# Optimization experiments

Hardware: AMD Instinct MI355X
Metric: run time of the kernel (lower is better)

Reference implementation:

```python
import jax, jax.numpy as jnp
import numpy as np

B, H, W, DIM = 8, 128, 128, 96
MED = 2 * DIM            # med_channels
NS = 3                   # num_scales
SCTX = 48                # spatial context channels
RIN = DIM + SCTX         # reweight mlp input
RHID = int(0.25 * RIN)   # 36
ROUT = NS * MED          # 576
FH, FWH = H, W // 2 + 1  # rfft2 output grid
SCALE_HW = [(16, 9), (8, 4), (24, 13)]  # per-scale filter resolutions


def _cubic(t, a=-0.75):
    t = abs(t)
    if t <= 1.0:
        return (a + 2) * t ** 3 - (a + 3) * t ** 2 + 1.0
    if t < 2.0:
        return a * t ** 3 - 5 * a * t ** 2 + 8 * a * t - 4 * a
    return 0.0


def _resize_mat(old, new):
    # bicubic, align_corners=True, border replication (matches F.interpolate)
    M = np.zeros((new, old), dtype=np.float32)
    for j in range(new):
        s = j * (old - 1) / (new - 1) if new > 1 else 0.0
        f = int(np.floor(s))
        for k in range(-1, 3):
            M[j, min(max(f + k, 0), old - 1)] += _cubic(s - (f + k))
    return jnp.asarray(M)


def _soa(x, scale, bias):
    r = jnp.maximum(x, 0.0)
    return scale * r * r + bias


def setup_inputs() -> dict:
    key = jax.random.key(0)
    ks = jax.random.split(key, 10)
    inp = {
        "x": jax.random.normal(ks[0], (B, H, W, DIM), dtype=jnp.float32),
        "w1": jax.random.normal(ks[1], (MED, DIM), dtype=jnp.float32) * 0.02,
        "soa1_scale": jnp.ones((1,), jnp.float32),
        "soa1_bias": jnp.zeros((1,), jnp.float32),
        "cw0": jax.random.normal(ks[2], (SCALE_HW[0][0], SCALE_HW[0][1], MED, 2), dtype=jnp.float32) * 0.02,
        "cw1": jax.random.normal(ks[3], (SCALE_HW[1][0], SCALE_HW[1][1], MED, 2), dtype=jnp.float32) * 0.02,
        "cw2": jax.random.normal(ks[4], (SCALE_HW[2][0], SCALE_HW[2][1], MED, 2), dtype=jnp.float32) * 0.02,
        "sp_w": jax.random.normal(ks[5], (SCTX, DIM), dtype=jnp.float32) * 0.05,
        "bn_gamma": jnp.ones((SCTX,), jnp.float32),
        "bn_beta": jnp.zeros((SCTX,), jnp.float32),
        "bn_mean": jnp.zeros((SCTX,), jnp.float32),
        "bn_var": jnp.ones((SCTX,), jnp.float32),
        "fc1": jax.random.normal(ks[6], (RHID, RIN), dtype=jnp.float32) * 0.05,
        "mlp_scale": jnp.ones((1,), jnp.float32),
        "mlp_bias": jnp.zeros((1,), jnp.float32),
        "fc2": jax.random.normal(ks[7], (ROUT, RHID), dtype=jnp.float32) * 0.05,
        "w2": jax.random.normal(ks[8], (DIM, MED), dtype=jnp.float32) * 0.02,
    }
    return inp


def reference(x, w1, soa1_scale, soa1_bias, cw0, cw1, cw2, sp_w,
              bn_gamma, bn_beta, bn_mean, bn_var,
              fc1, mlp_scale, mlp_bias, fc2, w2):
    # pwconv1 + Soa act
    x_pre = _soa(jnp.einsum('bhwc,mc->bhwm', x, w1), soa1_scale, soa1_bias)
    # rfft2 over spatial dims (ortho) -> [B, FH, FWH, MED] complex64
    xf = jnp.fft.rfft2(x_pre.transpose(0, 3, 1, 2), axes=(2, 3), norm='ortho').transpose(0, 2, 3, 1)
    # resize each scale's complex weight to the fft grid (bicubic align_corners=True)
    filts = []
    for cw in (cw0, cw1, cw2):
        Rh = _resize_mat(cw.shape[0], FH)
        Rw = _resize_mat(cw.shape[1], FWH)
        t = jnp.einsum('Hh,hwmc->Hwmc', Rh, cw)
        t = jnp.einsum('Ww,Hwmc->HWmc', Rw, t)
        filts.append(jax.lax.complex(t[..., 0], t[..., 1]))
    filt = jnp.stack(filts)  # [NS, FH, FWH, MED] complex64
    # routing context: global channel mean + 1x1 conv / BN(eval) / relu / GAP
    gctx = x.mean(axis=(1, 2))  # [B, DIM]
    y = jnp.einsum('bhwc,sc->bhws', x, sp_w)
    y = (y - bn_mean) * jax.lax.rsqrt(bn_var + 1e-5) * bn_gamma + bn_beta
    sctx = jnp.maximum(y, 0.0).mean(axis=(1, 2))  # [B, SCTX]
    fused = jnp.concatenate([gctx, sctx], axis=1)  # [B, RIN]
    hmid = _soa(fused @ fc1.T, mlp_scale, mlp_bias)
    r = jax.nn.softmax((hmid @ fc2.T).reshape(-1, NS, MED), axis=1)  # [B, NS, MED]
    # routing-weighted combined filter + spectral multiply
    comb = jnp.einsum('shwm,bsm->bhwm', filt, r.astype(filt.dtype))
    xff = xf * comb
    xsp = jnp.fft.irfft2(xff.transpose(0, 3, 1, 2), s=(H, W), axes=(2, 3), norm='ortho').transpose(0, 2, 3, 1)
    # act2 is Identity; pwconv2
    return jnp.einsum('bhwm,cm->bhwc', xsp, w2)
```

## Files before the change

kernel.cpp:

```cpp
#include <hip/hip_runtime.h>
#include <math.h>

#define BB    8
#define HH    128
#define WW    128
#define DIM   96
#define MED   192
#define HWPX  16384
#define FWH   65
#define LSTR  67

#define P_OFF     0
#define P_SZ      (8*192*16384)
#define FILT_OFF  (P_OFF + P_SZ)
#define FILT_SZ   (3*192*128*65*2)
#define GS_OFF    (FILT_OFF + FILT_SZ)
#define SS_OFF    (GS_OFF + 768)
#define R_OFF     (SS_OFF + 384)
#define W1B_OFF   (R_OFF + 4608)
#define W2B_OFF   (W1B_OFF + 23040)

typedef __attribute__((ext_vector_type(8))) short short8_t;
typedef __attribute__((ext_vector_type(4))) float float4_t;

__device__ __forceinline__ unsigned short bf16_rne(float f){
  unsigned u = __float_as_uint(f);
  unsigned r = (u + 0x7FFFu + ((u>>16)&1u)) >> 16;
  return (unsigned short)r;
}
__device__ __forceinline__ float bf16_to_f(unsigned short h){
  return __uint_as_float(((unsigned)h) << 16);
}

__global__ __launch_bounds__(256) void k_prep(
    const float* __restrict__ w1, const float* __restrict__ sp_w,
    const float* __restrict__ w2,
    unsigned short* __restrict__ W1B, unsigned short* __restrict__ W2B)
{
  int tid = threadIdx.x + blockIdx.x*256;
  int nthr = 256*36;
  for (int i = tid; i < 2*3*15*512; i += nthr) {
    int j = i & 7, l = (i>>3) & 63;
    int nt = (i>>9) % 15, kc = ((i>>9)/15) % 3, term = i / (3*15*512);
    int r = nt*16 + (l&15);
    int c = kc*32 + (l>>4)*8 + j;
    float v = (r < 192) ? w1[r*96 + c] : sp_w[(r-192)*96 + c];
    unsigned short hi = bf16_rne(v);
    W1B[i] = (term==0) ? hi : bf16_rne(v - bf16_to_f(hi));
  }
  for (int i = tid; i < 2*6*6*512; i += nthr) {
    int j = i & 7, l = (i>>3) & 63;
    int nt = (i>>9) % 6, kc = ((i>>9)/6) % 6, term = i / (6*6*512);
    int cp = nt*16 + (l&15);
    int m  = kc*32 + (l>>4)*8 + j;
    float v = w2[cp*192 + m];
    unsigned short hi = bf16_rne(v);
    W2B[i] = (term==0) ? hi : bf16_rne(v - bf16_to_f(hi));
  }
}

__global__ __launch_bounds__(256) void k_pw1(
    const float* __restrict__ x, const unsigned short* __restrict__ W1B,
    const float* __restrict__ soa_scale, const float* __restrict__ soa_bias,
    const float* __restrict__ bn_gamma, const float* __restrict__ bn_beta,
    const float* __restrict__ bn_mean, const float* __restrict__ bn_var,
    float* __restrict__ P, float* __restrict__ gsum, float* __restrict__ ssum)
{
  __shared__ float red[4][144];
  __shared__ float bnA_s[48], bnB_s[48];
  int t = threadIdx.x;
  int lane = t & 63, wv = t >> 6;
  if (t < 48) {
    float a = bn_gamma[t] * rsqrtf(bn_var[t] + 1e-5f);
    bnA_s[t] = a; bnB_s[t] = bn_beta[t] - bn_mean[t]*a;
  }
  int px0 = blockIdx.x*64 + wv*16;
  int b = (blockIdx.x*64) >> 14;
  int pxl = px0 & 16383;
  int g = lane >> 4;

  float4_t acc[15];
  #pragma unroll
  for (int nt=0; nt<15; ++nt) acc[nt] = (float4_t){0.f,0.f,0.f,0.f};

  #pragma unroll
  for (int kc=0; kc<3; ++kc) {
    const float* xp = x + (size_t)(px0 + (lane&15))*96 + kc*32 + g*8;
    float4 v0 = *(const float4*)xp;
    float4 v1 = *(const float4*)(xp+4);
    float vv[8] = {v0.x,v0.y,v0.z,v0.w, v1.x,v1.y,v1.z,v1.w};
    #pragma unroll
    for (int j=0;j<8;j++){
      float s = vv[j];
      s += __shfl_xor(s, 1);
      s += __shfl_xor(s, 2);
      s += __shfl_xor(s, 4);
      s += __shfl_xor(s, 8);
      if ((lane & 15) == 0) red[wv][kc*32 + g*8 + j] = s;
    }
    short8_t Bh, Bl;
    #pragma unroll
    for (int j=0;j<8;j++){
      unsigned short h = bf16_rne(vv[j]);
      Bh[j] = (short)h;
      Bl[j] = (short)bf16_rne(vv[j] - bf16_to_f(h));
    }
    const short8_t* a_hi = (const short8_t*)(W1B + (size_t)(0*3+kc)*15*512) + lane;
    const short8_t* a_lo = (const short8_t*)(W1B + (size_t)(1*3+kc)*15*512) + lane;
    #pragma unroll
    for (int nt=0; nt<15; ++nt) {
      short8_t Ah = a_hi[nt*64];
      short8_t Al = a_lo[nt*64];
      acc[nt] = __builtin_amdgcn_mfma_f32_16x16x32_bf16(Ah, Bh, acc[nt], 0,0,0);
      acc[nt] = __builtin_amdgcn_mfma_f32_16x16x32_bf16(Ah, Bl, acc[nt], 0,0,0);
      acc[nt] = __builtin_amdgcn_mfma_f32_16x16x32_bf16(Al, Bh, acc[nt], 0,0,0);
    }
  }
  float sc = soa_scale[0], bi = soa_bias[0];
  #pragma unroll
  for (int nt=0; nt<12; ++nt) {
    #pragma unroll
    for (int q=0;q<4;q++){
      float d = acc[nt][q];
      float v = fmaxf(d, 0.f);
      d = sc*v*v + bi;
      int mp = nt*16 + g*4 + q;
      P[(size_t)(b*192 + mp)*HWPX + pxl + (lane&15)] = d;
    }
  }
  #pragma unroll
  for (int tile=0; tile<3; ++tile) {
    #pragma unroll
    for (int q=0;q<4;q++){
      int s = tile*16 + g*4 + q;
      float y = acc[12+tile][q];
      float v = fmaxf(bnA_s[s]*y + bnB_s[s], 0.f);
      v += __shfl_xor(v, 1);
      v += __shfl_xor(v, 2);
      v += __shfl_xor(v, 4);
      v += __shfl_xor(v, 8);
      if ((lane & 15) == 0) red[wv][96 + s] = v;
    }
  }
  __syncthreads();
  if (t < 144) {
    float s = red[0][t] + red[1][t] + red[2][t] + red[3][t];
    if (t < 96) atomicAdd(&gsum[b*96 + t], s);
    else        atomicAdd(&ssum[b*48 + (t-96)], s);
  }
}

__global__ __launch_bounds__(256) void k_pw2(
    const float* __restrict__ P, const unsigned short* __restrict__ W2B,
    float* __restrict__ out)
{
  int t = threadIdx.x;
  int lane = t & 63, wv = t >> 6;
  int px0 = blockIdx.x*64 + wv*16;
  int b = px0 >> 14;
  int pxl = px0 & 16383;

  float4_t acc[6];
  #pragma unroll
  for (int nt=0; nt<6; ++nt) acc[nt] = (float4_t){0.f,0.f,0.f,0.f};

  #pragma unroll
  for (int kc=0; kc<6; ++kc) {
    const float* ap = P + (size_t)(b*192 + kc*32 + (lane>>4)*8)*HWPX + pxl + (lane&15);
    short8_t Ah, Al;
    #pragma unroll
    for (int j=0;j<8;j++){
      float v = ap[(size_t)j*HWPX];
      unsigned short h = bf16_rne(v);
      Ah[j] = (short)h;
      Al[j] = (short)bf16_rne(v - bf16_to_f(h));
    }
    const short8_t* b_hi = (const short8_t*)(W2B + (size_t)(0*6+kc)*6*512) + lane;
    const short8_t* b_lo = (const short8_t*)(W2B + (size_t)(1*6+kc)*6*512) + lane;
    #pragma unroll
    for (int nt=0; nt<6; ++nt) {
      short8_t Bh = b_hi[nt*64];
      short8_t Bl = b_lo[nt*64];
      acc[nt] = __builtin_amdgcn_mfma_f32_16x16x32_bf16(Ah, Bh, acc[nt], 0,0,0);
      acc[nt] = __builtin_amdgcn_mfma_f32_16x16x32_bf16(Ah, Bl, acc[nt], 0,0,0);
      acc[nt] = __builtin_amdgcn_mfma_f32_16x16x32_bf16(Al, Bh, acc[nt], 0,0,0);
    }
  }
  #pragma unroll
  for (int nt=0; nt<6; ++nt) {
    #pragma unroll
    for (int q=0;q<4;q++){
      int px = px0 + (lane>>4)*4 + q;
      out[(size_t)px*96 + nt*16 + (lane&15)] = acc[nt][q];
    }
  }
}

__global__ __launch_bounds__(256) void k_route2(
    const float* __restrict__ gsum, const float* __restrict__ ssum,
    const float* __restrict__ fc1, const float* __restrict__ fc2,
    const float* __restrict__ mlp_scale, const float* __restrict__ mlp_bias,
    float* __restrict__ r_out)
{
  __shared__ float fused[144], hmid[36], rpre[576];
  int t = threadIdx.x, b = blockIdx.x;
  if (t < 96) fused[t] = gsum[b*96+t] * (1.f/16384.f);
  else if (t < 144) fused[t] = ssum[b*48 + (t-96)] * (1.f/16384.f);
  __syncthreads();
  if (t < 36) {
    float a = 0.f;
    for (int i=0;i<144;i++) a = fmaf(fused[i], fc1[t*144+i], a);
    float rr = fmaxf(a, 0.f);
    hmid[t] = mlp_scale[0]*rr*rr + mlp_bias[0];
  }
  __syncthreads();
  for (int o = t; o < 576; o += 256) {
    float a = 0.f;
    for (int j=0;j<36;j++) a = fmaf(hmid[j], fc2[o*36+j], a);
    rpre[o] = a;
  }
  __syncthreads();
  if (t < 192) {
    float v0 = rpre[t], v1 = rpre[192+t], v2 = rpre[384+t];
    float mx = fmaxf(v0, fmaxf(v1, v2));
    float e0 = expf(v0-mx), e1 = expf(v1-mx), e2 = expf(v2-mx);
    float inv = 1.f/(e0+e1+e2);
    r_out[(b*3+0)*192+t] = e0*inv;
    r_out[(b*3+1)*192+t] = e1*inv;
    r_out[(b*3+2)*192+t] = e2*inv;
  }
}

__device__ __forceinline__ float cubicw(float tt){
  float t = fabsf(tt), t2=t*t, t3=t2*t;
  if (t <= 1.f) return 1.25f*t3 - 2.25f*t2 + 1.f;
  if (t < 2.f)  return -0.75f*t3 + 3.75f*t2 - 6.f*t + 3.f;
  return 0.f;
}

__global__ __launch_bounds__(256) void k_filt(
    const float* __restrict__ cw0, const float* __restrict__ cw1,
    const float* __restrict__ cw2, float* __restrict__ filt)
{
  int bx = blockIdx.x; int s = bx >> 7; int fh = bx & 127;
  const float* cw = (s==0) ? cw0 : ((s==1) ? cw1 : cw2);
  int SH = (s==0) ? 16 : ((s==1) ? 8 : 24);
  int SW = (s==0) ? 9  : ((s==1) ? 4 : 13);
  float sh = fh * (float)(SH-1) / 127.f;
  int fh0 = (int)floorf(sh);
  float wh[4]; int ih[4];
  #pragma unroll
  for (int k=0;k<4;k++){
    int kk = fh0-1+k;
    wh[k] = cubicw(sh - (float)kk);
    ih[k] = min(max(kk,0), SH-1);
  }
  int t = threadIdx.x;
  for (int i = t; i < 192*65; i += 256) {
    int m = i / 65, fw = i % 65;
    float sw = fw * (float)(SW-1) / 64.f;
    int fw0 = (int)floorf(sw);
    float are=0.f, aim=0.f;
    #pragma unroll
    for (int kb=0;kb<4;kb++){
      int jj = fw0-1+kb;
      float wwb = cubicw(sw - (float)jj);
      int iw = min(max(jj,0), SW-1);
      #pragma unroll
      for (int ka=0;ka<4;ka++){
        const float* p = cw + (size_t)((ih[ka]*SW + iw)*192 + m)*2;
        float wgt = wh[ka]*wwb;
        are = fmaf(wgt, p[0], are);
        aim = fmaf(wgt, p[1], aim);
      }
    }
    *(float2*)&filt[ (size_t)(((s*192+m)*128 + fh)*65 + fw) * 2 ] = make_float2(are, aim);
  }
}

__device__ __forceinline__ float2 c_add(float2 a, float2 b){ return make_float2(a.x+b.x, a.y+b.y); }
__device__ __forceinline__ float2 c_sub(float2 a, float2 b){ return make_float2(a.x-b.x, a.y-b.y); }
__device__ __forceinline__ float2 c_mul(float2 a, float2 w){ return make_float2(a.x*w.x - a.y*w.y, a.x*w.y + a.y*w.x); }
__device__ __forceinline__ float2 c_mulc(float2 a, float2 w){ return make_float2(a.x*w.x + a.y*w.y, a.y*w.x - a.x*w.y); }

__device__ __forceinline__ void dif4(float2* S, const float2* TW,
    int a0, int a1, int a2, int a3, int t1, int t2, int t3)
{
  float2 x0=S[a0], x1=S[a1], x2=S[a2], x3=S[a3];
  float2 u = c_add(x0,x2), d0 = c_sub(x0,x2);
  float2 s = c_add(x1,x3), d1 = c_sub(x1,x3);
  float2 w = c_mul(d0, TW[t1]);
  float2 v = c_mul(d1, TW[t2]);
  float2 t3w = TW[t3];
  S[a0] = c_add(u,s);
  S[a1] = c_mul(c_sub(u,s), t3w);
  S[a2] = c_add(w,v);
  S[a3] = c_mul(c_sub(w,v), t3w);
}

__device__ __forceinline__ void dit4(float2* S, const float2* TW,
    int a0, int a1, int a2, int a3, int tA, int tB, int tC)
{
  float2 x0=S[a0], x1=S[a1], x2=S[a2], x3=S[a3];
  float2 wA = TW[tA];
  float2 x1t = c_mulc(x1, wA), x3t = c_mulc(x3, wA);
  float2 u = c_add(x0,x1t), v = c_sub(x0,x1t);
  float2 s = c_add(x2,x3t), w = c_sub(x2,x3t);
  float2 st = c_mulc(s, TW[tB]);
  float2 wt = c_mulc(w, TW[tC]);
  S[a0] = c_add(u, st);
  S[a2] = c_sub(u, st);
  S[a1] = c_add(v, wt);
  S[a3] = c_sub(v, wt);
}

__global__ __launch_bounds__(512, 4) void k_spectral(
    float* __restrict__ P, const float* __restrict__ filt, const float* __restrict__ r)
{
  __shared__ float2 S[128*LSTR];
  __shared__ float2 TW[64];
  int t = threadIdx.x;
  int bm = blockIdx.x;
  int b = bm & 7; int m = bm >> 3;
  float* plane = P + ((size_t)b*192 + m) * HWPX;

  if (t < 64) {
    float ang = -6.283185307179586477f * (float)t / 128.f;
    TW[t] = make_float2(cosf(ang), sinf(ang));
  }
  for (int it = 0; it < 8; ++it) {
    int idx = t + 512*it;
    int h = idx >> 5, j = idx & 31;
    float4 v = ((const float4*)plane)[idx];
    int base = h*LSTR + 2*j;
    S[base]   = make_float2(v.x, v.y);
    S[base+1] = make_float2(v.z, v.w);
  }
  float r0 = r[(b*3+0)*192+m];
  float r1 = r[(b*3+1)*192+m];
  float r2 = r[(b*3+2)*192+m];
  __syncthreads();

  #pragma unroll
  for (int ps = 0; ps < 3; ++ps) {
    const int lh = 5 - 2*ps;
    const int h1 = 1 << lh, h2 = h1 >> 1;
    for (int it = 0; it < 4; ++it) {
      int idx = t + 512*it;
      int g = idx & 15, row = idx >> 4;
      int k = g & (h2-1), blk = g >> (lh-1);
      int base = row*LSTR + blk*(2*h1) + k;
      dif4(S,TW, base, base+h2, base+h1, base+h1+h2,
           k << (6-lh), (k+h2) << (6-lh), k << (7-lh));
    }
    __syncthreads();
  }

  for (int it = 0; it < 9; ++it) {
    int idx = t + 512*it;
    if (idx < 128*33) {
      int row = idx & 127, k = idx >> 7;
      int base = row*LSTR;
      if (k == 0) {
        float2 z = S[base];
        S[base]    = make_float2(z.x + z.y, 0.f);
        S[base+64] = make_float2(z.x - z.y, 0.f);
      } else {
        int a = __brev((unsigned)k) >> 26;
        int bidx = __brev((unsigned)(64-k)) >> 26;
        float2 A = S[base+a], B = S[base+bidx];
        float sr_ = 0.5f*(A.x+B.x), si_ = 0.5f*(A.y-B.y);
        float dr  = 0.5f*(A.x-B.x), di  = 0.5f*(A.y+B.y);
        float2 w = TW[k];
        float tr = w.x*di + w.y*dr;
        float ti = -(w.x*dr - w.y*di);
        S[base+a]    = make_float2(sr_ + tr,  si_ + ti);
        S[base+bidx] = make_float2(sr_ - tr, -si_ + ti);
      }
    }
  }
  __syncthreads();

  #pragma unroll
  for (int ps = 0; ps < 3; ++ps) {
    const int lh = 6 - 2*ps;
    const int h1 = 1 << lh, h2 = h1 >> 1;
    for (int it = 0; it < 5; ++it) {
      int idx = t + 512*it;
      if (idx < 65*32) {
        int g = idx / 65, col = idx - g*65;
        int k = g & (h2-1), blk = g >> (lh-1);
        int p = blk*(2*h1) + k;
        dif4(S,TW, p*LSTR+col, (p+h2)*LSTR+col, (p+h1)*LSTR+col, (p+h1+h2)*LSTR+col,
             k << (6-lh), (k+h2) << (6-lh), k << (7-lh));
      }
    }
    __syncthreads();
  }
  for (int it = 0; it < 9; ++it) {
    int idx = t + 512*it;
    if (idx < 65*64) {
      int j = idx / 65, col = idx - j*65;
      int a0 = (2*j)*LSTR + col, a1 = a0 + LSTR;
      float2 u = S[a0], v = S[a1];
      S[a0] = c_add(u,v); S[a1] = c_sub(u,v);
    }
  }
  __syncthreads();

  {
    const float2* fb0 = (const float2*)filt + (size_t)(0*192+m)*8320;
    const float2* fb1 = (const float2*)filt + (size_t)(1*192+m)*8320;
    const float2* fb2 = (const float2*)filt + (size_t)(2*192+m)*8320;
    const float inv = 1.f/8192.f;
    for (int it = 0; it < 17; ++it) {
      int idx = t + 512*it;
      if (idx < 8320) {
        int fh = idx / 65, fw = idx - fh*65;
        float2 f0 = fb0[idx], f1 = fb1[idx], f2 = fb2[idx];
        float cr = (r0*f0.x + r1*f1.x + r2*f2.x) * inv;
        float ci = (r0*f0.y + r1*f1.y + r2*f2.y) * inv;
        int sh = __brev((unsigned)fh) >> 25;
        int sw = (fw == 64) ? 64 : (__brev((unsigned)fw) >> 26);
        int a = sh*LSTR + sw;
        float2 X = S[a];
        S[a] = make_float2(X.x*cr - X.y*ci, X.x*ci + X.y*cr);
      }
    }
  }
  __syncthreads();

  #pragma unroll
  for (int ps = 0; ps < 3; ++ps) {
    const int la = 2*ps;
    const int h = 1 << la;
    for (int it = 0; it < 5; ++it) {
      int idx = t + 512*it;
      if (idx < 65*32) {
        int g = idx / 65, col = idx - g*65;
        int k = g & (h-1), blk = g >> la;
        int p = blk*(4*h) + k;
        dit4(S,TW, p*LSTR+col, (p+h)*LSTR+col, (p+2*h)*LSTR+col, (p+3*h)*LSTR+col,
             k << (6-la), k << (5-la), (k+h) << (5-la));
      }
    }
    __syncthreads();
  }
  for (int it = 0; it < 9; ++it) {
    int idx = t + 512*it;
    if (idx < 65*64) {
      int k = idx / 65, col = idx - k*65;
      int a0 = k*LSTR + col, a1 = a0 + 64*LSTR;
      float2 u = S[a0], xv = S[a1];
      float2 xt = c_mulc(xv, TW[k]);
      S[a0] = c_add(u,xt); S[a1] = c_sub(u,xt);
    }
  }
  __syncthreads();

  for (int it = 0; it < 9; ++it) {
    int idx = t + 512*it;
    if (idx < 128*33) {
      int row = idx & 127, k = idx >> 7;
      int base = row*LSTR;
      if (k == 0) {
        float ar = S[base].x;
        float cr = S[base+64].x;
        S[base] = make_float2(0.5f*(ar+cr), 0.5f*(ar-cr));
      } else {
        int a = __brev((unsigned)k) >> 26;
        int bidx = __brev((unsigned)(64-k)) >> 26;
        float2 A = S[base+a], B = S[base+bidx];
        float sr_ = 0.5f*(A.x+B.x), si_ = 0.5f*(A.y-B.y);
        float dr  = 0.5f*(A.x-B.x), di  = 0.5f*(A.y+B.y);
        float2 w = TW[k];
        float tr2 = w.y*dr - w.x*di;
        float ti2 = w.x*dr + w.y*di;
        S[base+a]    = make_float2(sr_ + tr2,  si_ + ti2);
        S[base+bidx] = make_float2(sr_ - tr2, -si_ + ti2);
      }
    }
  }
  __syncthreads();

  #pragma unroll
  for (int ps = 0; ps < 3; ++ps) {
    const int la = 2*ps;
    const int h = 1 << la;
    for (int it = 0; it < 4; ++it) {
      int idx = t + 512*it;
      int g = idx & 15, row = idx >> 4;
      int k = g & (h-1), blk = g >> la;
      int base = row*LSTR + blk*(4*h) + k;
      dit4(S,TW, base, base+h, base+2*h, base+3*h,
           k << (6-la), k << (5-la), (k+h) << (5-la));
    }
    __syncthreads();
  }

  for (int it = 0; it < 8; ++it) {
    int idx = t + 512*it;
    int h = idx >> 5, j = idx & 31;
    int base = h*LSTR + 2*j;
    float2 z0 = S[base], z1 = S[base+1];
    float4 v; v.x = z0.x; v.y = z0.y; v.z = z1.x; v.w = z1.y;
    ((float4*)plane)[idx] = v;
  }
}

extern "C" void kernel_launch(void* const* d_in, const int* in_sizes, int n_in,
                              void* d_out, int out_size, void* d_ws, size_t ws_size,
                              hipStream_t stream) {
  const float* x          = (const float*)d_in[0];
  const float* w1         = (const float*)d_in[1];
  const float* soa1_scale = (const float*)d_in[2];
  const float* soa1_bias  = (const float*)d_in[3];
  const float* cw0        = (const float*)d_in[4];
  const float* cw1        = (const float*)d_in[5];
  const float* cw2        = (const float*)d_in[6];
  const float* sp_w       = (const float*)d_in[7];
  const float* bn_gamma   = (const float*)d_in[8];
  const float* bn_beta    = (const float*)d_in[9];
  const float* bn_mean    = (const float*)d_in[10];
  const float* bn_var     = (const float*)d_in[11];
  const float* fc1        = (const float*)d_in[12];
  const float* mlp_scale  = (const float*)d_in[13];
  const float* mlp_bias   = (const float*)d_in[14];
  const float* fc2        = (const float*)d_in[15];
  const float* w2         = (const float*)d_in[16];
  float* out = (float*)d_out;

  float* ws   = (float*)d_ws;
  float* P    = ws + P_OFF;
  float* filt = ws + FILT_OFF;
  float* gsum = ws + GS_OFF;
  float* ssum = ws + SS_OFF;
  float* rbuf = ws + R_OFF;
  unsigned short* W1B = (unsigned short*)(ws + W1B_OFF);
  unsigned short* W2B = (unsigned short*)(ws + W2B_OFF);

  hipMemsetAsync(gsum, 0, (768+384)*sizeof(float), stream);

  k_prep   <<<36,   256, 0, stream>>>(w1, sp_w, w2, W1B, W2B);
  k_pw1    <<<2048, 256, 0, stream>>>(x, W1B, soa1_scale, soa1_bias,
                                      bn_gamma, bn_beta, bn_mean, bn_var,
                                      P, gsum, ssum);
  k_route2 <<<8,    256, 0, stream>>>(gsum, ssum, fc1, fc2, mlp_scale, mlp_bias, rbuf);
  k_filt   <<<384,  256, 0, stream>>>(cw0, cw1, cw2, filt);
  k_spectral<<<1536,512, 0, stream>>>(P, filt, rbuf);
  k_pw2    <<<2048, 256, 0, stream>>>(P, W2B, out);
}
```

Baseline: 421.7 us.

## Assign rows/columns per wavefront to drop block barriers; prepermute filter layout

Row-FFT and column-FFT stages are remapped so each wavefront owns a fixed set of rows (or columns), which lets most __syncthreads between radix-4 passes be removed and relies on wavefront-lockstep execution instead. The k_filt kernel now writes the filter in the FFT's bit-reversed order, so the spectral multiply reads it contiguously with no scatter. The final radix-2 column stage is fused with that multiply, and the block-to-(b,m) mapping is reordered. Correctness depends on intra-wavefront ordering of LDS accesses, and each wave writes its own TW copy without a barrier, which risks hidden races.

```diff
diff --git a/kernel.cpp b/kernel.cpp
--- a/kernel.cpp
+++ b/kernel.cpp
@@ -242,7 +242,8 @@
     const float* __restrict__ cw0, const float* __restrict__ cw1,
     const float* __restrict__ cw2, float* __restrict__ filt)
 {
-  int bx = blockIdx.x; int s = bx >> 7; int fh = bx & 127;
+  int bx = blockIdx.x; int s = bx >> 7; int rr = bx & 127;
+  int fh = __brev((unsigned)rr) >> 25;
   const float* cw = (s==0) ? cw0 : ((s==1) ? cw1 : cw2);
   int SH = (s==0) ? 16 : ((s==1) ? 8 : 24);
   int SW = (s==0) ? 9  : ((s==1) ? 4 : 13);
@@ -257,7 +258,8 @@
   }
   int t = threadIdx.x;
   for (int i = t; i < 192*65; i += 256) {
-    int m = i / 65, fw = i % 65;
+    int m = i / 65, cc = i % 65;
+    int fw = (cc == 64) ? 64 : (__brev((unsigned)cc) >> 26);
     float sw = fw * (float)(SW-1) / 64.f;
     int fw0 = (int)floorf(sw);
     float are=0.f, aim=0.f;
@@ -274,7 +276,7 @@
         aim = fmaf(wgt, p[1], aim);
       }
     }
-    *(float2*)&filt[ (size_t)(((s*192+m)*128 + fh)*65 + fw) * 2 ] = make_float2(are, aim);
+    *(float2*)&filt[ (size_t)(((s*192+m)*128 + rr)*65 + cc) * 2 ] = make_float2(are, aim);
   }
 }
 
@@ -320,46 +322,51 @@
   __shared__ float2 S[128*LSTR];
   __shared__ float2 TW[64];
   int t = threadIdx.x;
-  int bm = blockIdx.x;
-  int b = bm & 7; int m = bm >> 3;
+  int lane = t & 63, wid = t >> 6;
+
+  int i = blockIdx.x;
+  int b = (i >> 3) & 7;
+  int m = (i & 7) * 24 + (i >> 6);
   float* plane = P + ((size_t)b*192 + m) * HWPX;
 
-  if (t < 64) {
-    float ang = -6.283185307179586477f * (float)t / 128.f;
-    TW[t] = make_float2(cosf(ang), sinf(ang));
-  }
+  {
+    float ang = -6.283185307179586477f * (float)lane / 128.f;
+    TW[lane] = make_float2(cosf(ang), sinf(ang));
+  }
+
   for (int it = 0; it < 8; ++it) {
-    int idx = t + 512*it;
-    int h = idx >> 5, j = idx & 31;
-    float4 v = ((const float4*)plane)[idx];
-    int base = h*LSTR + 2*j;
+    int row = 4*wid + (lane>>4) + 32*(it>>1);
+    int j   = (it&1)*16 + (lane&15);
+    float4 v = ((const float4*)plane)[row*32 + j];
+    int base = row*LSTR + 2*j;
     S[base]   = make_float2(v.x, v.y);
     S[base+1] = make_float2(v.z, v.w);
   }
   float r0 = r[(b*3+0)*192+m];
   float r1 = r[(b*3+1)*192+m];
   float r2 = r[(b*3+2)*192+m];
-  __syncthreads();
 
   #pragma unroll
   for (int ps = 0; ps < 3; ++ps) {
     const int lh = 5 - 2*ps;
     const int h1 = 1 << lh, h2 = h1 >> 1;
+    #pragma unroll
     for (int it = 0; it < 4; ++it) {
-      int idx = t + 512*it;
-      int g = idx & 15, row = idx >> 4;
+      int g = lane & 15;
+      int row = 4*wid + (lane>>4) + 32*it;
       int k = g & (h2-1), blk = g >> (lh-1);
       int base = row*LSTR + blk*(2*h1) + k;
       dif4(S,TW, base, base+h2, base+h1, base+h1+h2,
            k << (6-lh), (k+h2) << (6-lh), k << (7-lh));
     }
-    __syncthreads();
   }
 
   for (int it = 0; it < 9; ++it) {
-    int idx = t + 512*it;
-    if (idx < 128*33) {
-      int row = idx & 127, k = idx >> 7;
+    int loc = lane + 64*it;
+    if (loc < 528) {
+      int rl = loc / 33;
+      int k  = loc - 33*rl;
+      int row = 4*wid + (rl&3) + 32*(rl>>2);
       int base = row*LSTR;
       if (k == 0) {
         float2 z = S[base];
@@ -371,9 +378,9 @@
         float2 A = S[base+a], B = S[base+bidx];
         float sr_ = 0.5f*(A.x+B.x), si_ = 0.5f*(A.y-B.y);
         float dr  = 0.5f*(A.x-B.x), di  = 0.5f*(A.y+B.y);
-        float2 w = TW[k];
-        float tr = w.x*di + w.y*dr;
-        float ti = -(w.x*dr - w.y*di);
+        float2 wq = TW[k];
+        float tr = wq.x*di + wq.y*dr;
+        float ti = -(wq.x*dr - wq.y*di);
         S[base+a]    = make_float2(sr_ + tr,  si_ + ti);
         S[base+bidx] = make_float2(sr_ - tr, -si_ + ti);
       }
@@ -386,24 +393,15 @@
     const int lh = 6 - 2*ps;
     const int h1 = 1 << lh, h2 = h1 >> 1;
     for (int it = 0; it < 5; ++it) {
-      int idx = t + 512*it;
-      if (idx < 65*32) {
-        int g = idx / 65, col = idx - g*65;
+      int wv = wid + 8*it;
+      int col = 2*wv + (lane>>5);
+      if (wv < 33 && col < 65) {
+        int g = lane & 31;
         int k = g & (h2-1), blk = g >> (lh-1);
         int p = blk*(2*h1) + k;
         dif4(S,TW, p*LSTR+col, (p+h2)*LSTR+col, (p+h1)*LSTR+col, (p+h1+h2)*LSTR+col,
              k << (6-lh), (k+h2) << (6-lh), k << (7-lh));
       }
-    }
-    __syncthreads();
-  }
-  for (int it = 0; it < 9; ++it) {
-    int idx = t + 512*it;
-    if (idx < 65*64) {
-      int j = idx / 65, col = idx - j*65;
-      int a0 = (2*j)*LSTR + col, a1 = a0 + LSTR;
-      float2 u = S[a0], v = S[a1];
-      S[a0] = c_add(u,v); S[a1] = c_sub(u,v);
     }
   }
   __syncthreads();
@@ -413,18 +411,22 @@
     const float2* fb1 = (const float2*)filt + (size_t)(1*192+m)*8320;
     const float2* fb2 = (const float2*)filt + (size_t)(2*192+m)*8320;
     const float inv = 1.f/8192.f;
-    for (int it = 0; it < 17; ++it) {
+    for (int it = 0; it < 9; ++it) {
       int idx = t + 512*it;
-      if (idx < 8320) {
-        int fh = idx / 65, fw = idx - fh*65;
-        float2 f0 = fb0[idx], f1 = fb1[idx], f2 = fb2[idx];
-        float cr = (r0*f0.x + r1*f1.x + r2*f2.x) * inv;
-        float ci = (r0*f0.y + r1*f1.y + r2*f2.y) * inv;
-        int sh = __brev((unsigned)fh) >> 25;
-        int sw = (fw == 64) ? 64 : (__brev((unsigned)fw) >> 26);
-        int a = sh*LSTR + sw;
-        float2 X = S[a];
-        S[a] = make_float2(X.x*cr - X.y*ci, X.x*ci + X.y*cr);
+      if (idx < 65*64) {
+        int j = idx / 65, col = idx - j*65;
+        int i0 = (2*j)*65 + col;
+        int a0 = (2*j)*LSTR + col, a1 = a0 + LSTR;
+        float2 u = S[a0], v = S[a1];
+        float2 e = c_add(u,v), o = c_sub(u,v);
+        float2 f00=fb0[i0],    f10=fb1[i0],    f20=fb2[i0];
+        float2 f01=fb0[i0+65], f11=fb1[i0+65], f21=fb2[i0+65];
+        float cr0 = (r0*f00.x + r1*f10.x + r2*f20.x) * inv;
+        float ci0 = (r0*f00.y + r1*f10.y + r2*f20.y) * inv;
+        float cr1 = (r0*f01.x + r1*f11.x + r2*f21.x) * inv;
+        float ci1 = (r0*f01.y + r1*f11.y + r2*f21.y) * inv;
+        S[a0] = make_float2(e.x*cr0 - e.y*ci0, e.x*ci0 + e.y*cr0);
+        S[a1] = make_float2(o.x*cr1 - o.y*ci1, o.x*ci1 + o.y*cr1);
       }
     }
   }
@@ -435,33 +437,39 @@
     const int la = 2*ps;
     const int h = 1 << la;
     for (int it = 0; it < 5; ++it) {
-      int idx = t + 512*it;
-      if (idx < 65*32) {
-        int g = idx / 65, col = idx - g*65;
+      int wv = wid + 8*it;
+      int col = 2*wv + (lane>>5);
+      if (wv < 33 && col < 65) {
+        int g = lane & 31;
         int k = g & (h-1), blk = g >> la;
         int p = blk*(4*h) + k;
         dit4(S,TW, p*LSTR+col, (p+h)*LSTR+col, (p+2*h)*LSTR+col, (p+3*h)*LSTR+col,
              k << (6-la), k << (5-la), (k+h) << (5-la));
       }
     }
-    __syncthreads();
-  }
+  }
+  for (int it = 0; it < 5; ++it) {
+    int wv = wid + 8*it;
+    int col = 2*wv + (lane>>5);
+    if (wv < 33 && col < 65) {
+      #pragma unroll
+      for (int rep = 0; rep < 2; ++rep) {
+        int k = (lane&31) + 32*rep;
+        int a0 = k*LSTR + col, a1 = a0 + 64*LSTR;
+        float2 u = S[a0], xv = S[a1];
+        float2 xt = c_mulc(xv, TW[k]);
+        S[a0] = c_add(u,xt); S[a1] = c_sub(u,xt);
+      }
+    }
+  }
+  __syncthreads();
+
   for (int it = 0; it < 9; ++it) {
-    int idx = t + 512*it;
-    if (idx < 65*64) {
-      int k = idx / 65, col = idx - k*65;
-      int a0 = k*LSTR + col, a1 = a0 + 64*LSTR;
-      float2 u = S[a0], xv = S[a1];
-      float2 xt = c_mulc(xv, TW[k]);
-      S[a0] = c_add(u,xt); S[a1] = c_sub(u,xt);
-    }
-  }
-  __syncthreads();
-
-  for (int it = 0; it < 9; ++it) {
-    int idx = t + 512*it;
-    if (idx < 128*33) {
-      int row = idx & 127, k = idx >> 7;
+    int loc = lane + 64*it;
+    if (loc < 528) {
+      int rl = loc / 33;
+      int k  = loc - 33*rl;
+      int row = 4*wid + (rl&3) + 32*(rl>>2);
       int base = row*LSTR;
       if (k == 0) {
         float ar = S[base].x;
@@ -473,38 +481,37 @@
         float2 A = S[base+a], B = S[base+bidx];
         float sr_ = 0.5f*(A.x+B.x), si_ = 0.5f*(A.y-B.y);
         float dr  = 0.5f*(A.x-B.x), di  = 0.5f*(A.y+B.y);
-        float2 w = TW[k];
-        float tr2 = w.y*dr - w.x*di;
-        float ti2 = w.x*dr + w.y*di;
+        float2 wq = TW[k];
+        float tr2 = wq.y*dr - wq.x*di;
+        float ti2 = wq.x*dr + wq.y*di;
         S[base+a]    = make_float2(sr_ + tr2,  si_ + ti2);
         S[base+bidx] = make_float2(sr_ - tr2, -si_ + ti2);
       }
     }
   }
-  __syncthreads();
 
   #pragma unroll
   for (int ps = 0; ps < 3; ++ps) {
     const int la = 2*ps;
     const int h = 1 << la;
+    #pragma unroll
     for (int it = 0; it < 4; ++it) {
-      int idx = t + 512*it;
-      int g = idx & 15, row = idx >> 4;
+      int g = lane & 15;
+      int row = 4*wid + (lane>>4) + 32*it;
       int k = g & (h-1), blk = g >> la;
       int base = row*LSTR + blk*(4*h) + k;
       dit4(S,TW, base, base+h, base+2*h, base+3*h,
            k << (6-la), k << (5-la), (k+h) << (5-la));
     }
-    __syncthreads();
   }
 
   for (int it = 0; it < 8; ++it) {
-    int idx = t + 512*it;
-    int h = idx >> 5, j = idx & 31;
-    int base = h*LSTR + 2*j;
+    int row = 4*wid + (lane>>4) + 32*(it>>1);
+    int j   = (it&1)*16 + (lane&15);
+    int base = row*LSTR + 2*j;
     float2 z0 = S[base], z1 = S[base+1];
     float4 v; v.x = z0.x; v.y = z0.y; v.z = z1.x; v.w = z1.y;
-    ((float4*)plane)[idx] = v;
+    ((float4*)plane)[row*32 + j] = v;
   }
 }
 
```

Measured after the change: 532.6 us. +26.3%, slower.
